# Optimization experiments

Hardware: AMD Instinct MI355X
Metric: run time of the kernel (lower is better)

Reference implementation:

```python
import jax, jax.numpy as jnp
import numpy as np

NS = 16384   # N*S support examples
NQ = 16384   # N*Q query examples
D = 64       # embedding dim
N_CLASSES = 64


def setup_inputs() -> dict:
    key = jax.random.key(0)
    k1, k2, k3 = jax.random.split(key, 3)
    support_embeddings = jax.random.normal(k1, (NS, D), dtype=jnp.float32)
    query_embeddings = jax.random.normal(k2, (NQ, D), dtype=jnp.float32)
    labels = jax.random.randint(k3, (NS,), 0, N_CLASSES)
    support_labels_onehot = jax.nn.one_hot(labels, N_CLASSES, dtype=jnp.float32)
    return {
        "support_embeddings": support_embeddings,
        "query_embeddings": query_embeddings,
        "support_labels_onehot": support_labels_onehot,
    }


def reference(support_embeddings, query_embeddings, support_labels_onehot):
    # Pairwise L2 distance via ||q||^2 + ||s||^2 - 2 q.s (same math as
    # tf.norm(q[:,None,:] - s[None,:,:], axis=2) without the [NQ,NS,D] blowup).
    sq_s = jnp.sum(support_embeddings * support_embeddings, axis=-1)  # [NS]
    sq_q = jnp.sum(query_embeddings * query_embeddings, axis=-1)      # [NQ]
    cross = jnp.einsum('qd,sd->qs', query_embeddings, support_embeddings)  # [NQ,NS]
    d2 = sq_q[:, None] + sq_s[None, :] - 2.0 * cross
    distance = jnp.sqrt(jnp.maximum(d2, 0.0))
    # top_k(-distance, k=1) == first argmin along support axis
    indices = jnp.argmin(distance, axis=1)                 # [NQ]
    labels_x = jnp.argmax(support_labels_onehot, axis=1)   # [NS]
    labels_pred = labels_x[indices]                        # [NQ] gather
    num_classes = support_labels_onehot.shape[1]
    labels_prob = jax.nn.one_hot(labels_pred, num_classes, dtype=support_labels_onehot.dtype)
    return labels_prob
```

## Files before the change

### kernel.cpp

```cpp
#include <hip/hip_runtime.h>


#define NTOT   16384
#define DIM    64
#define EPS_COEF 0.004f
#define EPS_ABS  0.05f
#define CINIT_COEF (-0.499f)
#define FLT_BIG 3.4e38f

typedef __attribute__((ext_vector_type(8))) short short8;
typedef __attribute__((ext_vector_type(4))) float float4v;

__device__ __forceinline__ ushort f16_bits(float x) {
  union { _Float16 f; ushort u; } c;
  c.f = (_Float16)x;
  return c.u;
}

__device__ __forceinline__ void pin8(short8& v) {
  asm volatile("" : "+v"(v));
}

__global__ __launch_bounds__(256) void k_prep(
    const float* __restrict__ S, const float* __restrict__ Q,
    ushort* __restrict__ Sh, ushort* __restrict__ Qh,
    float* __restrict__ sqS, float* __restrict__ sqQ,
    float* __restrict__ sqSc, float* __restrict__ S_T) {
  __shared__ float tile[64][65];
  const int tid = threadIdx.x;
  const bool isS = blockIdx.x < 256;
  const int rbase = (blockIdx.x & 255) * 64;
  const float* __restrict__ src = isS ? S : Q;
  ushort* __restrict__ dh = isS ? Sh : Qh;

  const int tx = tid & 63;
  const int ty = tid >> 6;
#pragma unroll
  for (int i = 0; i < 16; ++i) {
    const int r = i * 4 + ty;
    tile[r][tx] = src[(size_t)(rbase + r) * DIM + tx];
  }
  __syncthreads();

  if (isS) {
#pragma unroll
    for (int i = 0; i < 16; ++i) {
      const int d = i * 4 + ty;
      S_T[(size_t)d * NTOT + rbase + tx] = tile[tx][d];
    }
  }

  const int panel = tid >> 6;
  const int half = (tid >> 5) & 1;
  const int slot0 = (tid & 31) * 2;
#pragma unroll
  for (int ss = 0; ss < 2; ++ss) {
    const int s = slot0 + ss;
    const int m = s & 15;
    const int q8 = s >> 4;
    const int row = panel * 16 + m;
    const int kb = half * 32 + q8 * 8;
    short8 hv;
#pragma unroll
    for (int j = 0; j < 8; ++j) hv[j] = (short)f16_bits(tile[row][kb + j]);
    const size_t goff =
        (size_t)((rbase >> 4) + panel) * 1024 + (size_t)half * 512 + (size_t)s * 8;
    *(short8*)&dh[goff] = hv;
  }

  if (tid < 64) {
    float acc = 0.0f;
#pragma unroll
    for (int d = 0; d < DIM; ++d) {
      const float v = tile[tid][d];
      acc = fmaf(v, v, acc);
    }
    if (isS) {
      sqS[rbase + tid] = acc;
      sqSc[rbase + tid] = CINIT_COEF * acc;
    } else {
      sqQ[rbase + tid] = acc;
    }
  }
}


#define MFMA16F(A, B, C) __builtin_amdgcn_mfma_f32_16x16x32_f16(A, B, C, 0, 0, 0)

#define STEP_COMPUTE(H0, H1, SQ)                                           \
  do {                                                                     \
    float4v cinit;                                                         \
    cinit[0] = SQ.x;                                                       \
    cinit[1] = SQ.y;                                                       \
    cinit[2] = SQ.z;                                                       \
    cinit[3] = SQ.w;                                                       \
    _Pragma("unroll")                                                      \
    for (int t = 0; t < 4; ++t) {                                          \
      float4v a = MFMA16F(H0, qh[t][0], cinit);                            \
      a = MFMA16F(H1, qh[t][1], a);                                        \
             \
      bmr[t] = fmaxf(fmaxf(fmaxf(a[0], a[1]), a[2]), fmaxf(a[3], bmr[t])); \
    }                                                                      \
  } while (0)

template <int BST>
__global__ __launch_bounds__(256, 3) void k_phaseA(
    const ushort* __restrict__ Sh, const ushort* __restrict__ Qh,
    const float* __restrict__ sqSc, float* __restrict__ bmin) {
  constexpr int NSB = NTOT / (16 * BST);
  const int tid = threadIdx.x;
  const int l = tid & 63;
  const int w = tid >> 6;
  const int lm = l & 15;
  const int lq = l >> 4;
  const int split = blockIdx.x;
  const int qbase = blockIdx.y * 64;
  const int sbase = split * 2048 + w * 512;

  short8 qh[4][2];
#pragma unroll
  for (int t = 0; t < 4; ++t) {
    const size_t pb = (size_t)((qbase >> 4) + t) * 1024 + (size_t)l * 8;
    qh[t][0] = *(const short8*)&Qh[pb];
    qh[t][1] = *(const short8*)&Qh[pb + 512];
  }
#pragma unroll
  for (int t = 0; t < 4; ++t) {
    pin8(qh[t][0]);
    pin8(qh[t][1]);
  }

  const ushort* pSh = Sh + (size_t)(sbase >> 4) * 1024 + (size_t)l * 8;
  const float* psq = sqSc + sbase + lq * 4;

  short8 h0a = *(const short8*)(pSh);
  short8 h1a = *(const short8*)(pSh + 512);
  float4 sqa = *(const float4*)(psq);
  short8 h0b = *(const short8*)(pSh + 1024);
  short8 h1b = *(const short8*)(pSh + 1024 + 512);
  float4 sqb = *(const float4*)(psq + 16);

  float bmr[4] = {-FLT_BIG, -FLT_BIG, -FLT_BIG, -FLT_BIG};

  for (int st = 0; st < 32; st += 2) {
    STEP_COMPUTE(h0a, h1a, sqa);
    if (st + 2 < 32) {
      const int off = (st + 2) * 1024;
      h0a = *(const short8*)(pSh + off);
      h1a = *(const short8*)(pSh + off + 512);
      sqa = *(const float4*)(psq + (st + 2) * 16);
    }
    STEP_COMPUTE(h0b, h1b, sqb);
    if (st + 3 < 32) {
      const int off = (st + 3) * 1024;
      h0b = *(const short8*)(pSh + off);
      h1b = *(const short8*)(pSh + off + 512);
      sqb = *(const float4*)(psq + (st + 3) * 16);
    }
    if (((st + 1) & (BST - 1)) == (BST - 1)) {
      const int gb = split * (128 / BST) + w * (32 / BST) + ((st + 1) / BST);
#pragma unroll
      for (int t = 0; t < 4; ++t) {
        float v = bmr[t];
        v = fmaxf(v, __shfl_xor(v, 16, 64));
        v = fmaxf(v, __shfl_xor(v, 32, 64));
        if (lq == 0) bmin[(size_t)(qbase + t * 16 + lm) * NSB + gb] = -2.0f * v;
        bmr[t] = -FLT_BIG;
      }
    }
  }
}

template <int SBLK>
__global__ __launch_bounds__(256, 3) void k_phaseB(
    const float* __restrict__ S_T,
    const float* __restrict__ Q,
    const float* __restrict__ sqS, const float* __restrict__ sqQ,
    const float* __restrict__ bmin,
    const float* __restrict__ onehot, float* __restrict__ out) {
  constexpr int NSB = NTOT / SBLK;
  constexpr int NB64 = NSB / 64;
  constexpr int SPL = SBLK / 64;

  __shared__ float sQrow[4][64];
  __shared__ unsigned long long smask[4][NB64];
  __shared__ float sbk[4][4];
  __shared__ int sbi[4][4];

  const int lane = threadIdx.x & 63;
  const int w = threadIdx.x >> 6;
  const int q = blockIdx.x * 4 + w;

  if (lane < 16)
    *(float4*)&sQrow[w][lane * 4] = *(const float4*)&Q[(size_t)q * DIM + lane * 4];

  const float eps = EPS_COEF * sqQ[q] + EPS_ABS;

  float bv[NB64];
#pragma unroll
  for (int j = 0; j < NB64; ++j) bv[j] = bmin[(size_t)q * NSB + j * 64 + lane];
  float m = bv[0];
#pragma unroll
  for (int j = 1; j < NB64; ++j) m = fminf(m, bv[j]);
#pragma unroll
  for (int d = 1; d < 64; d <<= 1) m = fminf(m, __shfl_xor(m, d, 64));
  const float thr = m + eps;

#pragma unroll
  for (int j = 0; j < NB64; ++j) {
    const unsigned long long msk = __ballot(bv[j] <= thr);
    if (lane == 0) smask[w][j] = msk;
  }
  __syncthreads();

  int idx = 0;
  for (int qq = 0; qq < 4; ++qq) {
    float bkq = FLT_BIG;
    int biq = 0;
    for (int j = 0; j < NB64; ++j) {
      unsigned long long msk = smask[qq][j];
      while (msk) {
        const int b = j * 64 + (__ffsll((long long)msk) - 1);
        msk &= msk - 1;
        if ((idx++ & 3) != w) continue;
        const int s0 = b * SBLK + lane * SPL;
        if (SPL == 2) {
          float a0 = 0.f, a1 = 0.f;
#pragma unroll
          for (int h = 0; h < 2; ++h) {
            float2 x[32];
#pragma unroll
            for (int d = 0; d < 32; ++d)
              x[d] = *(const float2*)&S_T[(size_t)(h * 32 + d) * NTOT + s0];
            __builtin_amdgcn_sched_barrier(0);
#pragma unroll
            for (int d = 0; d < 32; ++d) {
              const float qd = sQrow[qq][h * 32 + d];
              a0 = fmaf(qd, x[d].x, a0);
              a1 = fmaf(qd, x[d].y, a1);
            }
            __builtin_amdgcn_sched_barrier(0);
          }
          const float2 sq2 = *(const float2*)&sqS[s0];
          const float k0 = fmaf(-2.f, a0, sq2.x);
          const float k1 = fmaf(-2.f, a1, sq2.y);
          bool u;
          u = k0 < bkq; bkq = u ? k0 : bkq; biq = u ? s0 : biq;
          u = k1 < bkq; bkq = u ? k1 : bkq; biq = u ? (s0 + 1) : biq;
        } else {
          float a0 = 0.f, a1 = 0.f, a2 = 0.f, a3 = 0.f;
#pragma unroll
          for (int hh = 0; hh < 4; ++hh) {
            float4 x[16];
#pragma unroll
            for (int d = 0; d < 16; ++d)
              x[d] = *(const float4*)&S_T[(size_t)(hh * 16 + d) * NTOT + s0];
            __builtin_amdgcn_sched_barrier(0);
#pragma unroll
            for (int d = 0; d < 16; ++d) {
              const float qd = sQrow[qq][hh * 16 + d];
              a0 = fmaf(qd, x[d].x, a0);
              a1 = fmaf(qd, x[d].y, a1);
              a2 = fmaf(qd, x[d].z, a2);
              a3 = fmaf(qd, x[d].w, a3);
            }
            __builtin_amdgcn_sched_barrier(0);
          }
          const float4 sq4 = *(const float4*)&sqS[s0];
          const float k0 = fmaf(-2.f, a0, sq4.x);
          const float k1 = fmaf(-2.f, a1, sq4.y);
          const float k2 = fmaf(-2.f, a2, sq4.z);
          const float k3 = fmaf(-2.f, a3, sq4.w);
          bool u;
          u = k0 < bkq; bkq = u ? k0 : bkq; biq = u ? s0 : biq;
          u = k1 < bkq; bkq = u ? k1 : bkq; biq = u ? (s0 + 1) : biq;
          u = k2 < bkq; bkq = u ? k2 : bkq; biq = u ? (s0 + 2) : biq;
          u = k3 < bkq; bkq = u ? k3 : bkq; biq = u ? (s0 + 3) : biq;
        }
      }
    }
#pragma unroll
    for (int d = 1; d < 64; d <<= 1) {
      const float ok = __shfl_xor(bkq, d, 64);
      const int oi = __shfl_xor(biq, d, 64);
      const bool u = (ok < bkq) || (ok == bkq && oi < biq);
      bkq = u ? ok : bkq;
      biq = u ? oi : biq;
    }
    if (lane == 0) { sbk[qq][w] = bkq; sbi[qq][w] = biq; }
  }
  __syncthreads();

  float fk = sbk[w][0];
  int fi = sbi[w][0];
#pragma unroll
  for (int ww = 1; ww < 4; ++ww) {
    const float ok = sbk[w][ww];
    const int oi = sbi[w][ww];
    const bool u = (ok < fk) || (ok == fk && oi < fi);
    fk = u ? ok : fk;
    fi = u ? oi : fi;
  }

  const float ov = onehot[(size_t)fi * 64 + lane];
  const unsigned long long lmask = __ballot(ov > 0.5f);
  const int label = __ffsll((long long)lmask) - 1;
  out[(size_t)q * 64 + lane] = (lane == label) ? 1.0f : 0.0f;
}

extern "C" void kernel_launch(void* const* d_in, const int* in_sizes, int n_in,
                              void* d_out, int out_size, void* d_ws, size_t ws_size,
                              hipStream_t stream) {
  const float* S = (const float*)d_in[0];
  const float* Q = (const float*)d_in[1];
  const float* OH = (const float*)d_in[2];
  float* out = (float*)d_out;

  char* ws = (char*)d_ws;
  ushort* Sh = (ushort*)ws;
  ushort* Qh = (ushort*)(ws + (2u << 20));
  float* S_T = (float*)(ws + (4u << 20));
  float* sqS = (float*)(ws + (8u << 20));
  float* sqQ = (float*)(ws + (8u << 20) + (64u << 10));
  float* sqSc = (float*)(ws + (8u << 20) + (128u << 10));
  float* bmin = (float*)(ws + (8u << 20) + (192u << 10));

  k_prep<<<dim3(512), 256, 0, stream>>>(S, Q, Sh, Qh, sqS, sqQ, sqSc, S_T);

  if (ws_size >= (17u << 20)) {
    k_phaseA<8><<<dim3(8, NTOT / 64), 256, 0, stream>>>(Sh, Qh, sqSc, bmin);
    k_phaseB<128><<<dim3(NTOT / 4), 256, 0, stream>>>(S_T, Q, sqS, sqQ,
                                                      bmin, OH, out);
  } else {
    k_phaseA<16><<<dim3(8, NTOT / 64), 256, 0, stream>>>(Sh, Qh, sqSc, bmin);
    k_phaseB<256><<<dim3(NTOT / 4), 256, 0, stream>>>(S_T, Q, sqS, sqQ,
                                                      bmin, OH, out);
  }
  (void)in_sizes; (void)n_in; (void)out_size; (void)ws_size;
}
```

Measured before the change: 148.3 us.

## Fuse prep, phaseA and phaseB into one persistent cooperative kernel

Merges the three kernel launches into a single cooperative persistent kernel that loops over work units and separates the phases with grid-wide syncs, sharing one LDS buffer between the prep tile and the phaseB scratch. The aim is to remove launch gaps and inter-kernel drain/fill between stages. It also drops the sched_barrier hints in phaseB's inner loops, leaving load/FMA scheduling to the compiler. Risks are grid-sync overhead, a grid size capped by occupancy that serialises work units, and register pressure or occupancy changes from merging all bodies into one kernel.

```diff
diff --git a/kernel.cpp b/kernel.cpp
--- a/kernel.cpp
+++ b/kernel.cpp
@@ -1,4 +1,5 @@
 #include <hip/hip_runtime.h>
+#include <hip/hip_cooperative_groups.h>
 
 
 #define NTOT   16384
@@ -8,6 +9,8 @@
 #define CINIT_COEF (-0.499f)
 #define FLT_BIG 3.4e38f
 
+namespace cg = cooperative_groups;
+
 typedef __attribute__((ext_vector_type(8))) short short8;
 typedef __attribute__((ext_vector_type(4))) float float4v;
 
@@ -21,15 +24,15 @@
   asm volatile("" : "+v"(v));
 }
 
-__global__ __launch_bounds__(256) void k_prep(
-    const float* __restrict__ S, const float* __restrict__ Q,
+__device__ __forceinline__ void prep_body(
+    int u, const float* __restrict__ S, const float* __restrict__ Q,
     ushort* __restrict__ Sh, ushort* __restrict__ Qh,
     float* __restrict__ sqS, float* __restrict__ sqQ,
-    float* __restrict__ sqSc, float* __restrict__ S_T) {
-  __shared__ float tile[64][65];
+    float* __restrict__ sqSc, float* __restrict__ S_T,
+    float (*tile)[65]) {
   const int tid = threadIdx.x;
-  const bool isS = blockIdx.x < 256;
-  const int rbase = (blockIdx.x & 255) * 64;
+  const bool isS = u < 256;
+  const int rbase = (u & 255) * 64;
   const float* __restrict__ src = isS ? S : Q;
   ushort* __restrict__ dh = isS ? Sh : Qh;
 
@@ -82,6 +85,7 @@
       sqQ[rbase + tid] = acc;
     }
   }
+  __syncthreads();
 }
 
 
@@ -104,7 +108,8 @@
   } while (0)
 
 template <int BST>
-__global__ __launch_bounds__(256, 3) void k_phaseA(
+__device__ __forceinline__ void phaseA_body(
+    int split, int qbase,
     const ushort* __restrict__ Sh, const ushort* __restrict__ Qh,
     const float* __restrict__ sqSc, float* __restrict__ bmin) {
   constexpr int NSB = NTOT / (16 * BST);
@@ -113,8 +118,6 @@
   const int w = tid >> 6;
   const int lm = l & 15;
   const int lq = l >> 4;
-  const int split = blockIdx.x;
-  const int qbase = blockIdx.y * 64;
   const int sbase = split * 2048 + w * 512;
 
   short8 qh[4][2];
@@ -172,27 +175,32 @@
 }
 
 template <int SBLK>
-__global__ __launch_bounds__(256, 3) void k_phaseB(
-    const float* __restrict__ S_T,
-    const float* __restrict__ Q,
+struct BShare {
+  static constexpr int NB64 = (NTOT / SBLK) / 64;
+  float sQrow[4][64];
+  unsigned long long smask[4][NB64];
+  float sbk[4][4];
+  int sbi[4][4];
+};
+
+template <int SBLK>
+__device__ __forceinline__ void phaseB_body(
+    int ublk, const float* __restrict__ S_T, const float* __restrict__ Q,
     const float* __restrict__ sqS, const float* __restrict__ sqQ,
-    const float* __restrict__ bmin,
-    const float* __restrict__ onehot, float* __restrict__ out) {
+    const float* __restrict__ bmin, const float* __restrict__ onehot,
+    float* __restrict__ out, BShare<SBLK>& sh) {
   constexpr int NSB = NTOT / SBLK;
   constexpr int NB64 = NSB / 64;
   constexpr int SPL = SBLK / 64;
 
-  __shared__ float sQrow[4][64];
-  __shared__ unsigned long long smask[4][NB64];
-  __shared__ float sbk[4][4];
-  __shared__ int sbi[4][4];
-
   const int lane = threadIdx.x & 63;
   const int w = threadIdx.x >> 6;
-  const int q = blockIdx.x * 4 + w;
+  const int q = ublk * 4 + w;
+
+  __syncthreads();
 
   if (lane < 16)
-    *(float4*)&sQrow[w][lane * 4] = *(const float4*)&Q[(size_t)q * DIM + lane * 4];
+    *(float4*)&sh.sQrow[w][lane * 4] = *(const float4*)&Q[(size_t)q * DIM + lane * 4];
 
   const float eps = EPS_COEF * sqQ[q] + EPS_ABS;
 
@@ -209,7 +217,7 @@
 #pragma unroll
   for (int j = 0; j < NB64; ++j) {
     const unsigned long long msk = __ballot(bv[j] <= thr);
-    if (lane == 0) smask[w][j] = msk;
+    if (lane == 0) sh.smask[w][j] = msk;
   }
   __syncthreads();
 
@@ -218,7 +226,7 @@
     float bkq = FLT_BIG;
     int biq = 0;
     for (int j = 0; j < NB64; ++j) {
-      unsigned long long msk = smask[qq][j];
+      unsigned long long msk = sh.smask[qq][j];
       while (msk) {
         const int b = j * 64 + (__ffsll((long long)msk) - 1);
         msk &= msk - 1;
@@ -232,14 +240,12 @@
 #pragma unroll
             for (int d = 0; d < 32; ++d)
               x[d] = *(const float2*)&S_T[(size_t)(h * 32 + d) * NTOT + s0];
-            __builtin_amdgcn_sched_barrier(0);
 #pragma unroll
             for (int d = 0; d < 32; ++d) {
-              const float qd = sQrow[qq][h * 32 + d];
+              const float qd = sh.sQrow[qq][h * 32 + d];
               a0 = fmaf(qd, x[d].x, a0);
               a1 = fmaf(qd, x[d].y, a1);
             }
-            __builtin_amdgcn_sched_barrier(0);
           }
           const float2 sq2 = *(const float2*)&sqS[s0];
           const float k0 = fmaf(-2.f, a0, sq2.x);
@@ -255,16 +261,14 @@
 #pragma unroll
             for (int d = 0; d < 16; ++d)
               x[d] = *(const float4*)&S_T[(size_t)(hh * 16 + d) * NTOT + s0];
-            __builtin_amdgcn_sched_barrier(0);
 #pragma unroll
             for (int d = 0; d < 16; ++d) {
-              const float qd = sQrow[qq][hh * 16 + d];
+              const float qd = sh.sQrow[qq][hh * 16 + d];
               a0 = fmaf(qd, x[d].x, a0);
               a1 = fmaf(qd, x[d].y, a1);
               a2 = fmaf(qd, x[d].z, a2);
               a3 = fmaf(qd, x[d].w, a3);
             }
-            __builtin_amdgcn_sched_barrier(0);
           }
           const float4 sq4 = *(const float4*)&sqS[s0];
           const float k0 = fmaf(-2.f, a0, sq4.x);
@@ -287,16 +291,16 @@
       bkq = u ? ok : bkq;
       biq = u ? oi : biq;
     }
-    if (lane == 0) { sbk[qq][w] = bkq; sbi[qq][w] = biq; }
+    if (lane == 0) { sh.sbk[qq][w] = bkq; sh.sbi[qq][w] = biq; }
   }
   __syncthreads();
 
-  float fk = sbk[w][0];
-  int fi = sbi[w][0];
+  float fk = sh.sbk[w][0];
+  int fi = sh.sbi[w][0];
 #pragma unroll
   for (int ww = 1; ww < 4; ++ww) {
-    const float ok = sbk[w][ww];
-    const int oi = sbi[w][ww];
+    const float ok = sh.sbk[w][ww];
+    const int oi = sh.sbi[w][ww];
     const bool u = (ok < fk) || (ok == fk && oi < fi);
     fk = u ? ok : fk;
     fi = u ? oi : fi;
@@ -306,6 +310,57 @@
   const unsigned long long lmask = __ballot(ov > 0.5f);
   const int label = __ffsll((long long)lmask) - 1;
   out[(size_t)q * 64 + lane] = (lane == label) ? 1.0f : 0.0f;
+}
+
+template <int BST>
+__global__ __launch_bounds__(256, 3) void k_fused(
+    const float* __restrict__ S, const float* __restrict__ Q,
+    const float* __restrict__ OH, float* __restrict__ out,
+    ushort* __restrict__ Sh, ushort* __restrict__ Qh,
+    float* __restrict__ sqS, float* __restrict__ sqQ,
+    float* __restrict__ sqSc, float* __restrict__ S_T,
+    float* __restrict__ bmin) {
+  constexpr int SBLK = 16 * BST;
+  __shared__ __align__(16) char smraw[sizeof(float) * 64 * 65];
+  static_assert(sizeof(BShare<SBLK>) <= sizeof(float) * 64 * 65, "lds");
+  float (*tile)[65] = reinterpret_cast<float(*)[65]>(smraw);
+  BShare<SBLK>* bs = reinterpret_cast<BShare<SBLK>*>(smraw);
+
+  const int G = gridDim.x;
+  for (int u = blockIdx.x; u < 512; u += G)
+    prep_body(u, S, Q, Sh, Qh, sqS, sqQ, sqSc, S_T, tile);
+  cg::this_grid().sync();
+  for (int u = blockIdx.x; u < 2048; u += G)
+    phaseA_body<BST>(u & 7, (u >> 3) * 64, Sh, Qh, sqSc, bmin);
+  cg::this_grid().sync();
+  for (int u = blockIdx.x; u < NTOT / 4; u += G)
+    phaseB_body<SBLK>(u, S_T, Q, sqS, sqQ, bmin, OH, out, *bs);
+}
+
+__global__ __launch_bounds__(256) void k_prep(
+    const float* __restrict__ S, const float* __restrict__ Q,
+    ushort* __restrict__ Sh, ushort* __restrict__ Qh,
+    float* __restrict__ sqS, float* __restrict__ sqQ,
+    float* __restrict__ sqSc, float* __restrict__ S_T) {
+  __shared__ float tile[64][65];
+  prep_body(blockIdx.x, S, Q, Sh, Qh, sqS, sqQ, sqSc, S_T, tile);
+}
+
+template <int BST>
+__global__ __launch_bounds__(256, 3) void k_phaseA(
+    const ushort* __restrict__ Sh, const ushort* __restrict__ Qh,
+    const float* __restrict__ sqSc, float* __restrict__ bmin) {
+  phaseA_body<BST>(blockIdx.x, blockIdx.y * 64, Sh, Qh, sqSc, bmin);
+}
+
+template <int SBLK>
+__global__ __launch_bounds__(256, 3) void k_phaseB(
+    const float* __restrict__ S_T, const float* __restrict__ Q,
+    const float* __restrict__ sqS, const float* __restrict__ sqQ,
+    const float* __restrict__ bmin, const float* __restrict__ onehot,
+    float* __restrict__ out) {
+  __shared__ BShare<SBLK> sh;
+  phaseB_body<SBLK>(blockIdx.x, S_T, Q, sqS, sqQ, bmin, onehot, out, sh);
 }
 
 extern "C" void kernel_launch(void* const* d_in, const int* in_sizes, int n_in,
@@ -325,16 +380,43 @@
   float* sqSc = (float*)(ws + (8u << 20) + (128u << 10));
   float* bmin = (float*)(ws + (8u << 20) + (192u << 10));
 
-  k_prep<<<dim3(512), 256, 0, stream>>>(S, Q, Sh, Qh, sqS, sqQ, sqSc, S_T);
-
-  if (ws_size >= (17u << 20)) {
-    k_phaseA<8><<<dim3(8, NTOT / 64), 256, 0, stream>>>(Sh, Qh, sqSc, bmin);
-    k_phaseB<128><<<dim3(NTOT / 4), 256, 0, stream>>>(S_T, Q, sqS, sqQ,
-                                                      bmin, OH, out);
-  } else {
-    k_phaseA<16><<<dim3(8, NTOT / 64), 256, 0, stream>>>(Sh, Qh, sqSc, bmin);
-    k_phaseB<256><<<dim3(NTOT / 4), 256, 0, stream>>>(S_T, Q, sqS, sqQ,
-                                                      bmin, OH, out);
+  const bool big = ws_size >= (17u << 20);
+
+  int nb = 0;
+  hipError_t oe;
+  if (big)
+    oe = hipOccupancyMaxActiveBlocksPerMultiprocessor(&nb, k_fused<8>, 256, 0);
+  else
+    oe = hipOccupancyMaxActiveBlocksPerMultiprocessor(&nb, k_fused<16>, 256, 0);
+  bool done = false;
+  if (oe == hipSuccess && nb >= 1) {
+    int G = nb * 256;
+    if (G > 2048) G = 2048;
+    void* args[] = {(void*)&S, (void*)&Q, (void*)&OH, (void*)&out,
+                    (void*)&Sh, (void*)&Qh, (void*)&sqS, (void*)&sqQ,
+                    (void*)&sqSc, (void*)&S_T, (void*)&bmin};
+    hipError_t le;
+    if (big)
+      le = hipLaunchCooperativeKernel(k_fused<8>, dim3(G), dim3(256), args, 0,
+                                      stream);
+    else
+      le = hipLaunchCooperativeKernel(k_fused<16>, dim3(G), dim3(256), args, 0,
+                                      stream);
+    done = (le == hipSuccess);
+    if (!done) (void)hipGetLastError();
+  }
+
+  if (!done) {
+    k_prep<<<dim3(512), 256, 0, stream>>>(S, Q, Sh, Qh, sqS, sqQ, sqSc, S_T);
+    if (big) {
+      k_phaseA<8><<<dim3(8, NTOT / 64), 256, 0, stream>>>(Sh, Qh, sqSc, bmin);
+      k_phaseB<128><<<dim3(NTOT / 4), 256, 0, stream>>>(S_T, Q, sqS, sqQ,
+                                                        bmin, OH, out);
+    } else {
+      k_phaseA<16><<<dim3(8, NTOT / 64), 256, 0, stream>>>(Sh, Qh, sqSc, bmin);
+      k_phaseB<256><<<dim3(NTOT / 4), 256, 0, stream>>>(S_T, Q, sqS, sqQ,
+                                                        bmin, OH, out);
+    }
   }
   (void)in_sizes; (void)n_in; (void)out_size; (void)ws_size;
 }
```

New measurement: 314.8 us. 112% more time.

## Stage support panels in LDS via async global_load_lds and share across query waves

Applied to the files above, without the earlier changes.

Phase A is reorganized so each block covers 256 queries (64 per wave) and a 512-row support slice. Support fp16 panels and their norms are double-buffered into shared memory with global_load_lds, so all four waves reuse the same staged tile instead of each wave streaming its own support rows from global memory. Launch bounds rise to 4 blocks per CU and the grid is reshaped to match. The sched_barrier hints in phase B are also removed. The cost is two LDS buffers and a block barrier per chunk.

```diff
diff --git a/kernel.cpp b/kernel.cpp
--- a/kernel.cpp
+++ b/kernel.cpp
@@ -87,35 +87,23 @@
 
 #define MFMA16F(A, B, C) __builtin_amdgcn_mfma_f32_16x16x32_f16(A, B, C, 0, 0, 0)
 
-#define STEP_COMPUTE(H0, H1, SQ)                                           \
-  do {                                                                     \
-    float4v cinit;                                                         \
-    cinit[0] = SQ.x;                                                       \
-    cinit[1] = SQ.y;                                                       \
-    cinit[2] = SQ.z;                                                       \
-    cinit[3] = SQ.w;                                                       \
-    _Pragma("unroll")                                                      \
-    for (int t = 0; t < 4; ++t) {                                          \
-      float4v a = MFMA16F(H0, qh[t][0], cinit);                            \
-      a = MFMA16F(H1, qh[t][1], a);                                        \
-             \
-      bmr[t] = fmaxf(fmaxf(fmaxf(a[0], a[1]), a[2]), fmaxf(a[3], bmr[t])); \
-    }                                                                      \
-  } while (0)
-
 template <int BST>
-__global__ __launch_bounds__(256, 3) void k_phaseA(
+__global__ __launch_bounds__(256, 4) void k_phaseA(
     const ushort* __restrict__ Sh, const ushort* __restrict__ Qh,
     const float* __restrict__ sqSc, float* __restrict__ bmin) {
   constexpr int NSB = NTOT / (16 * BST);
+  constexpr int SBLK = 16 * BST;
+  __shared__ ushort spanel[2][4096];
+  __shared__ float ssq[2][64];
+
   const int tid = threadIdx.x;
   const int l = tid & 63;
   const int w = tid >> 6;
   const int lm = l & 15;
   const int lq = l >> 4;
   const int split = blockIdx.x;
-  const int qbase = blockIdx.y * 64;
-  const int sbase = split * 2048 + w * 512;
+  const int qbase = blockIdx.y * 256 + w * 64;
+  const int sbase = split * 512;
 
   short8 qh[4][2];
 #pragma unroll
@@ -130,35 +118,50 @@
     pin8(qh[t][1]);
   }
 
-  const ushort* pSh = Sh + (size_t)(sbase >> 4) * 1024 + (size_t)l * 8;
-  const float* psq = sqSc + sbase + lq * 4;
-
-  short8 h0a = *(const short8*)(pSh);
-  short8 h1a = *(const short8*)(pSh + 512);
-  float4 sqa = *(const float4*)(psq);
-  short8 h0b = *(const short8*)(pSh + 1024);
-  short8 h1b = *(const short8*)(pSh + 1024 + 512);
-  float4 sqb = *(const float4*)(psq + 16);
+  auto stage = [&](int c, int b) {
+    const ushort* gs = Sh + ((size_t)(split * 32 + c * 4)) * 1024 +
+                       (size_t)w * 1024 + (size_t)l * 8;
+    ushort* ls = &spanel[b][w * 1024];
+    __builtin_amdgcn_global_load_lds(
+        (const __attribute__((address_space(1))) void*)(const void*)gs,
+        (__attribute__((address_space(3))) void*)(void*)ls, 16, 0, 0);
+    __builtin_amdgcn_global_load_lds(
+        (const __attribute__((address_space(1))) void*)(const void*)(gs + 512),
+        (__attribute__((address_space(3))) void*)(void*)(ls + 512), 16, 0, 0);
+    if (tid < 16)
+      *(float4*)&ssq[b][tid * 4] =
+          *(const float4*)&sqSc[sbase + c * 64 + tid * 4];
+  };
 
   float bmr[4] = {-FLT_BIG, -FLT_BIG, -FLT_BIG, -FLT_BIG};
 
-  for (int st = 0; st < 32; st += 2) {
-    STEP_COMPUTE(h0a, h1a, sqa);
-    if (st + 2 < 32) {
-      const int off = (st + 2) * 1024;
-      h0a = *(const short8*)(pSh + off);
-      h1a = *(const short8*)(pSh + off + 512);
-      sqa = *(const float4*)(psq + (st + 2) * 16);
-    }
-    STEP_COMPUTE(h0b, h1b, sqb);
-    if (st + 3 < 32) {
-      const int off = (st + 3) * 1024;
-      h0b = *(const short8*)(pSh + off);
-      h1b = *(const short8*)(pSh + off + 512);
-      sqb = *(const float4*)(psq + (st + 3) * 16);
-    }
-    if (((st + 1) & (BST - 1)) == (BST - 1)) {
-      const int gb = split * (128 / BST) + w * (32 / BST) + ((st + 1) / BST);
+  stage(0, 0);
+  __syncthreads();
+
+  for (int c = 0; c < 8; ++c) {
+    const int b = c & 1;
+    if (c + 1 < 8) stage(c + 1, b ^ 1);
+
+#pragma unroll
+    for (int st = 0; st < 4; ++st) {
+      const short8 h0 = *(const short8*)&spanel[b][st * 1024 + l * 8];
+      const short8 h1 = *(const short8*)&spanel[b][st * 1024 + 512 + l * 8];
+      const float4 sqv = *(const float4*)&ssq[b][st * 16 + lq * 4];
+      float4v cinit;
+      cinit[0] = sqv.x;
+      cinit[1] = sqv.y;
+      cinit[2] = sqv.z;
+      cinit[3] = sqv.w;
+#pragma unroll
+      for (int t = 0; t < 4; ++t) {
+        float4v a = MFMA16F(h0, qh[t][0], cinit);
+        a = MFMA16F(h1, qh[t][1], a);
+        bmr[t] = fmaxf(fmaxf(fmaxf(a[0], a[1]), a[2]), fmaxf(a[3], bmr[t]));
+      }
+    }
+
+    if ((((c + 1) * 4) & (BST - 1)) == 0) {
+      const int gb = split * (512 / SBLK) + ((c + 1) * 64 / SBLK) - 1;
 #pragma unroll
       for (int t = 0; t < 4; ++t) {
         float v = bmr[t];
@@ -168,6 +171,7 @@
         bmr[t] = -FLT_BIG;
       }
     }
+    __syncthreads();
   }
 }
 
@@ -232,14 +236,12 @@
 #pragma unroll
             for (int d = 0; d < 32; ++d)
               x[d] = *(const float2*)&S_T[(size_t)(h * 32 + d) * NTOT + s0];
-            __builtin_amdgcn_sched_barrier(0);
 #pragma unroll
             for (int d = 0; d < 32; ++d) {
               const float qd = sQrow[qq][h * 32 + d];
               a0 = fmaf(qd, x[d].x, a0);
               a1 = fmaf(qd, x[d].y, a1);
             }
-            __builtin_amdgcn_sched_barrier(0);
           }
           const float2 sq2 = *(const float2*)&sqS[s0];
           const float k0 = fmaf(-2.f, a0, sq2.x);
@@ -255,7 +257,6 @@
 #pragma unroll
             for (int d = 0; d < 16; ++d)
               x[d] = *(const float4*)&S_T[(size_t)(hh * 16 + d) * NTOT + s0];
-            __builtin_amdgcn_sched_barrier(0);
 #pragma unroll
             for (int d = 0; d < 16; ++d) {
               const float qd = sQrow[qq][hh * 16 + d];
@@ -264,7 +265,6 @@
               a2 = fmaf(qd, x[d].z, a2);
               a3 = fmaf(qd, x[d].w, a3);
             }
-            __builtin_amdgcn_sched_barrier(0);
           }
           const float4 sq4 = *(const float4*)&sqS[s0];
           const float k0 = fmaf(-2.f, a0, sq4.x);
@@ -328,11 +328,11 @@
   k_prep<<<dim3(512), 256, 0, stream>>>(S, Q, Sh, Qh, sqS, sqQ, sqSc, S_T);
 
   if (ws_size >= (17u << 20)) {
-    k_phaseA<8><<<dim3(8, NTOT / 64), 256, 0, stream>>>(Sh, Qh, sqSc, bmin);
+    k_phaseA<8><<<dim3(32, NTOT / 256), 256, 0, stream>>>(Sh, Qh, sqSc, bmin);
     k_phaseB<128><<<dim3(NTOT / 4), 256, 0, stream>>>(S_T, Q, sqS, sqQ,
                                                       bmin, OH, out);
   } else {
-    k_phaseA<16><<<dim3(8, NTOT / 64), 256, 0, stream>>>(Sh, Qh, sqSc, bmin);
+    k_phaseA<16><<<dim3(32, NTOT / 256), 256, 0, stream>>>(Sh, Qh, sqSc, bmin);
     k_phaseB<256><<<dim3(NTOT / 4), 256, 0, stream>>>(S_T, Q, sqS, sqQ,
                                                       bmin, OH, out);
   }
```

Measured after the change: 145.8 us. About the same (-1.7%).
